# Kernel tuning notes

Measured on AMD Instinct MI355X. Metric: run time of the kernel, lower is better.

## Reference

```python
import jax, jax.numpy as jnp
import numpy as np

# scaled DeepSeek-V2-style config
B, S, D, H, L = 1, 2048, 1024, 16, 2
E, K, I, SI, V = 8, 2, 512, 1024, 32000
Dh = D // H
IGNORE_IDX = -100


def setup_inputs() -> dict:
    key = jax.random.key(0)
    ks = jax.random.split(key, 18)
    f = lambda k, sh: jax.random.normal(k, sh, jnp.float32) * 0.02
    return {
        "src_tokens": jax.random.randint(ks[0], (B, S), 0, V, jnp.int32),
        "target": jax.random.randint(ks[1], (B, S), 0, V, jnp.int32),
        "embed": f(ks[2], (V, D)),
        "Wq": f(ks[3], (L, D, D)),
        "Wk": f(ks[4], (L, D, D)),
        "Wv": f(ks[5], (L, D, D)),
        "Wo": f(ks[6], (L, D, D)),
        "ln1": jnp.ones((L, D), jnp.float32),
        "ln2": jnp.ones((L, D), jnp.float32),
        "gate_w": f(ks[7], (L, E, D)),
        "gate_projs": f(ks[8], (L, E, I, D)),
        "up_projs": f(ks[9], (L, E, I, D)),
        "down_projs": f(ks[10], (L, E, D, I)),
        "sg": f(ks[11], (L, SI, D)),
        "su": f(ks[12], (L, SI, D)),
        "sd": f(ks[13], (L, D, SI)),
        "final_ln": jnp.ones((D,), jnp.float32),
        "lm_head": f(ks[14], (V, D)),
    }


def _rms(x, w, eps=1e-6):
    return x * jax.lax.rsqrt(jnp.mean(x * x, axis=-1, keepdims=True) + eps) * w


def _rot_half(x):
    x1, x2 = jnp.split(x, 2, axis=-1)
    return jnp.concatenate([-x2, x1], axis=-1)


def reference(src_tokens, target, embed, Wq, Wk, Wv, Wo, ln1, ln2, gate_w,
              gate_projs, up_projs, down_projs, sg, su, sd, final_ln, lm_head):
    # rotary tables [1,S,1,Dh]
    inv_freq = 1.0 / (10000.0 ** (jnp.arange(0, Dh, 2, dtype=jnp.float32) / Dh))
    ang = jnp.arange(S, dtype=jnp.float32)[:, None] * inv_freq[None, :]
    emb = jnp.concatenate([ang, ang], axis=-1)
    cos = jnp.cos(emb)[None, :, None, :]
    sin = jnp.sin(emb)[None, :, None, :]
    causal = jnp.tril(jnp.ones((S, S), bool))
    scale = 1.0 / float(np.sqrt(Dh))

    h = embed[src_tokens]  # [B,S,D]
    for l in range(L):
        x = _rms(h, ln1[l])
        q = (x @ Wq[l].T).reshape(B, S, H, Dh)
        k = (x @ Wk[l].T).reshape(B, S, H, Dh)
        v = (x @ Wv[l].T).reshape(B, S, H, Dh)
        q = q * cos + _rot_half(q) * sin
        k = k * cos + _rot_half(k) * sin
        sc = jnp.einsum('bqhd,bkhd->bhqk', q, k) * scale
        sc = jnp.where(causal, sc, -1e9)
        a = jax.nn.softmax(sc, axis=-1)
        o = jnp.einsum('bhqk,bkhd->bqhd', a, v).reshape(B, S, D)
        h = h + o @ Wo[l].T
        # DeepSeek-V2 MoE: softmax gate -> top-k combine over stacked experts
        x = _rms(h, ln2[l])
        probs = jax.nn.softmax(x @ gate_w[l].T, axis=-1)  # [B,S,E]
        topv, topi = jax.lax.top_k(probs, K)
        comb = (jax.nn.one_hot(topi, E, dtype=x.dtype) * topv[..., None]).sum(axis=2)  # [B,S,E]
        g = jnp.einsum('bsd,eid->bsei', x, gate_projs[l])
        u = jnp.einsum('bsd,eid->bsei', x, up_projs[l])
        act = jax.nn.silu(g) * u * comb[..., None]  # [B,S,E,I]
        routed = jnp.einsum('bsei,edi->bsd', act, down_projs[l])
        shared = (jax.nn.silu(x @ sg[l].T) * (x @ su[l].T)) @ sd[l].T
        h = h + routed + shared

    x = _rms(h, final_ln)
    logits = (x @ lm_head.T).reshape(-1, V).astype(jnp.float32)
    labels = target.reshape(-1)
    logp = jax.nn.log_softmax(logits, axis=-1)
    valid = labels != IGNORE_IDX
    safe = jnp.where(valid, labels, 0)
    nll = -jnp.take_along_axis(logp, safe[:, None], axis=1)[:, 0]
    loss = jnp.sum(jnp.where(valid, nll, 0.0))
    return loss
```

## Files before the change

kernel.cpp:

```cpp
#include <hip/hip_runtime.h>
#include <hip/hip_bf16.h>

#define S 2048
#define D 1024
#define H 16
#define DH 64
#define LAYERS 2
#define E 8
#define I_DIM 512
#define SI 1024
#define V 32000
#define NSTRIP 125

typedef unsigned short ushort_t;
typedef __attribute__((ext_vector_type(8))) short short8;
typedef __attribute__((ext_vector_type(4))) float floatx4;

__device__ __forceinline__ float bf2f(ushort_t u) {
  union { unsigned i; float f; } x;
  x.i = ((unsigned)u) << 16;
  return x.f;
}
__device__ __forceinline__ ushort_t f2bf(float f) {
  union { float f; unsigned u; } x; x.f = f;
  unsigned r = x.u + 0x7FFFu + ((x.u >> 16) & 1u);
  return (ushort_t)(r >> 16);
}
__device__ __forceinline__ int pack2(float a, float b) {
  return (int)((unsigned)f2bf(a) | ((unsigned)f2bf(b) << 16));
}

__device__ __forceinline__ int xcd_swz(int bid, int nwg) {
  int q = nwg >> 3, r = nwg & 7;
  int x = bid & 7, o = bid >> 3;
  return (x < r ? x * (q + 1) : r * (q + 1) + (x - r) * q) + o;
}

__device__ __forceinline__ void gl_lds16(const ushort_t* g, ushort_t* l) {
  __builtin_amdgcn_global_load_lds((const __attribute__((address_space(1))) void*)g,
                                   (__attribute__((address_space(3))) void*)l, 16, 0, 0);
}

__global__ __launch_bounds__(256) void convert_k(const float* __restrict__ in,
                                                 ushort_t* __restrict__ out, int n8) {
  int i = blockIdx.x * 256 + threadIdx.x;
  if (i >= n8) return;
  const float4* p = (const float4*)in + (size_t)i * 2;
  float4 a = p[0], b = p[1];
  int4 pk = {pack2(a.x, a.y), pack2(a.z, a.w), pack2(b.x, b.y), pack2(b.z, b.w)};
  ((int4*)out)[i] = pk;
}

__global__ __launch_bounds__(256) void convert_ilv_k(const float* __restrict__ in,
                                                     ushort_t* __restrict__ out,
                                                     int n8, int off) {
  int i = blockIdx.x * 256 + threadIdx.x;
  if (i >= n8) return;
  int row = i >> 7;
  int c8 = i & 127;
  const float4* p = (const float4*)in + (size_t)i * 2;
  float4 a = p[0], b = p[1];
  int4 pk = {pack2(a.x, a.y), pack2(a.z, a.w), pack2(b.x, b.y), pack2(b.z, b.w)};
  ((int4*)(out + ((size_t)(2 * row + off)) * D))[c8] = pk;
}

__global__ __launch_bounds__(256) void embed_k(const int* __restrict__ tok,
                                               const float* __restrict__ emb,
                                               float* __restrict__ h) {
  int idx = blockIdx.x * 256 + threadIdx.x;
  if (idx >= S * D / 4) return;
  int s = idx >> 8;
  int d4 = idx & 255;
  int t = tok[s];
  float4 u = *(const float4*)(emb + (size_t)t * D + d4 * 4);
  *(float4*)(h + (size_t)s * D + d4 * 4) = u;
}

__global__ __launch_bounds__(256) void rmsnorm_k(const float* __restrict__ h,
                                                 const float* __restrict__ w,
                                                 ushort_t* __restrict__ xb) {
  int s = blockIdx.x, tid = threadIdx.x;
  __shared__ float red[256];
  float4 hv = *(const float4*)(h + (size_t)s * D + tid * 4);
  red[tid] = hv.x * hv.x + hv.y * hv.y + hv.z * hv.z + hv.w * hv.w;
  __syncthreads();
  for (int st = 128; st > 0; st >>= 1) {
    if (tid < st) red[tid] += red[tid + st];
    __syncthreads();
  }
  float inv = rsqrtf(red[0] * (1.0f / 1024.0f) + 1e-6f);
  float4 wv = *(const float4*)(w + tid * 4);
  int2 pk;
  pk.x = pack2(hv.x * inv * wv.x, hv.y * inv * wv.y);
  pk.y = pack2(hv.z * inv * wv.z, hv.w * inv * wv.w);
  *(int2*)(xb + (size_t)s * D + tid * 4) = pk;
}

template <int TM, int TN, int MODE, int EXPERT>
__global__ __launch_bounds__(256) void gbt_k(const ushort_t* __restrict__ A, int lda,
                                             const ushort_t* __restrict__ B, int ldb,
                                             void* __restrict__ Cv, int ldc, int K) {
  constexpr int WM = TM / 2, WN = TN / 2;
  constexpr int MT = WM / 16, NT = WN / 16;
  constexpr int CA = TM / 16, CB = TN / 16;
  __shared__ __align__(16) ushort_t As[TM * 32];
  __shared__ __align__(16) ushort_t Bs[TN * 32];
  int tid = threadIdx.x;
  int nwg = gridDim.x * gridDim.y;
  int sw = xcd_swz(blockIdx.x + gridDim.x * blockIdx.y, nwg);
  int bx = sw / gridDim.y, by = sw % gridDim.y;
  int n0 = bx * TN, m0 = by * TM;
  int w = tid >> 6, lane = tid & 63, quad = lane >> 4, l16 = lane & 15;
  int wm = (w >> 1) * WM, wn = (w & 1) * WN;
  int srow = lane >> 2, sko = (lane & 3) * 8;

  floatx4 acc[MT][NT];
#pragma unroll
  for (int mi = 0; mi < MT; mi++)
#pragma unroll
    for (int ni = 0; ni < NT; ni++)
      acc[mi][ni] = (floatx4){0.f, 0.f, 0.f, 0.f};

  for (int k0 = 0; k0 < K; k0 += 32) {
#pragma unroll
    for (int c = 0; c < CA; c += 4) {
      int ch = c + w;
      const ushort_t* gp = A + (size_t)(m0 + ch * 16 + srow) * lda + k0 + sko;
      gl_lds16(gp, As + ch * 512);
    }
#pragma unroll
    for (int c = 0; c < CB; c += 4) {
      int ch = c + w;
      const ushort_t* gp;
      if (EXPERT) {
        int kk = k0 + sko;
        int e = kk >> 9;
        gp = B + ((size_t)(e * D + n0 + ch * 16 + srow)) * I_DIM + (kk & 511);
      } else {
        gp = B + (size_t)(n0 + ch * 16 + srow) * ldb + k0 + sko;
      }
      gl_lds16(gp, Bs + ch * 512);
    }
    __syncthreads();
    short8 af[MT], bfv[NT];
#pragma unroll
    for (int mi = 0; mi < MT; mi++)
      af[mi] = *(const short8*)(As + (wm + mi * 16 + l16) * 32 + quad * 8);
#pragma unroll
    for (int ni = 0; ni < NT; ni++)
      bfv[ni] = *(const short8*)(Bs + (wn + ni * 16 + l16) * 32 + quad * 8);
#pragma unroll
    for (int mi = 0; mi < MT; mi++)
#pragma unroll
      for (int ni = 0; ni < NT; ni++)
        acc[mi][ni] = __builtin_amdgcn_mfma_f32_16x16x32_bf16(af[mi], bfv[ni],
                                                              acc[mi][ni], 0, 0, 0);
    __syncthreads();
  }
#pragma unroll
  for (int mi = 0; mi < MT; mi++) {
#pragma unroll
    for (int ni = 0; ni < NT; ni++) {
      int row_base = m0 + wm + mi * 16 + quad * 4;
      int col = n0 + wn + ni * 16 + l16;
#pragma unroll
      for (int r = 0; r < 4; r++) {
        if (MODE == 1) {
          ((ushort_t*)Cv)[(size_t)(row_base + r) * ldc + col] = f2bf(acc[mi][ni][r]);
        } else if (MODE == 3) {
          float g = acc[mi][ni][r];
          float u = __shfl_xor(g, 1);
          if (!(l16 & 1)) {
            float sig = 1.0f / (1.0f + __expf(-g));
            ((ushort_t*)Cv)[(size_t)(row_base + r) * ldc + (col >> 1)] =
                f2bf(g * sig * u);
          }
        } else {
          float* cp = (float*)Cv + (size_t)(row_base + r) * ldc + col;
          float val = acc[mi][ni][r];
          if (MODE == 2) val += *cp;
          *cp = val;
        }
      }
    }
  }
}

#define GBODY(T, VMSTR, DOSTAGE)                                              \
  {                                                                           \
    if (DOSTAGE) STAGE((T) + 1);                                              \
    asm volatile("s_waitcnt vmcnt(" VMSTR ")" ::: "memory");                  \
    __builtin_amdgcn_sched_barrier(0);                                        \
    __builtin_amdgcn_s_barrier();                                             \
    __builtin_amdgcn_sched_barrier(0);                                        \
    asm volatile("" ::: "memory");                                            \
    const ushort_t* bA = smem + ((T) & 1) * SLOT;                             \
    const ushort_t* bB = bA + TM2 * 32;                                       \
    short8 af[MT], bfv[4];                                                    \
    _Pragma("unroll") for (int mi = 0; mi < MT; mi++) {                       \
      int row = wm + mi * 16 + l16;                                           \
      af[mi] = *(const short8*)(bA + row * 32 + ((quad ^ ((row >> 1) & 3)) << 3)); \
    }                                                                         \
    _Pragma("unroll") for (int ni = 0; ni < 4; ni++) {                        \
      int row = wn + ni * 16 + l16;                                           \
      bfv[ni] = *(const short8*)(bB + row * 32 + ((quad ^ ((row >> 1) & 3)) << 3)); \
    }                                                                         \
    __builtin_amdgcn_s_setprio(1);                                            \
    _Pragma("unroll") for (int mi = 0; mi < MT; mi++)                         \
      _Pragma("unroll") for (int ni = 0; ni < 4; ni++)                        \
        acc[mi][ni] = __builtin_amdgcn_mfma_f32_16x16x32_bf16(                \
            af[mi], bfv[ni], acc[mi][ni], 0, 0, 0);                           \
    __builtin_amdgcn_s_setprio(0);                                            \
    __builtin_amdgcn_sched_barrier(0);                                        \
    __builtin_amdgcn_s_barrier();                                             \
    asm volatile("" ::: "memory");                                            \
  }

template <int TM2, int MODE>
__global__ __launch_bounds__(512, 2) void gemm256_k(
    const ushort_t* __restrict__ A, int lda,
    const ushort_t* __restrict__ B, int ldb,
    void* __restrict__ Cv, int ldc, int K,
    const int* __restrict__ target, float2* __restrict__ partial,
    float* __restrict__ tgt_l, const float* __restrict__ combp, int strip_base) {
  constexpr int MT = TM2 / 32;
  constexpr int SLOT = (TM2 + 256) * 32;
  constexpr int RA = TM2 / 128;
  __shared__ __align__(16) ushort_t smem[2 * SLOT];
  int tid = threadIdx.x;
  int wv = tid >> 6, lane = tid & 63, quad = lane >> 4, l16 = lane & 15;
  int wm = (wv >> 2) * (TM2 / 2), wn = (wv & 3) * 64;
  int nwg = gridDim.x * gridDim.y;
  int sw = xcd_swz(blockIdx.x + gridDim.x * blockIdx.y, nwg);
  int bx = sw / gridDim.y, by = sw % gridDim.y;
  int m0 = by * TM2, n0 = bx * 256;
  int NT = K / 32;

  floatx4 acc[MT][4];
#pragma unroll
  for (int mi = 0; mi < MT; mi++)
#pragma unroll
    for (int ni = 0; ni < 4; ni++) acc[mi][ni] = (floatx4){0.f, 0.f, 0.f, 0.f};

  auto STAGE = [&](int t) {
    int b = t & 1, k0 = t * 32;
    ushort_t* ba = smem + b * SLOT;
#pragma unroll
    for (int ra = 0; ra < RA; ra++) {
      int Pb = ra * 8192 + tid * 16;
      int row = Pb >> 6;
      int kq = ((Pb >> 4) & 3) ^ ((row >> 1) & 3);
      gl_lds16(A + (size_t)(m0 + row) * lda + k0 + kq * 8,
               ba + ((ra * 8192 + wv * 1024) >> 1));
    }
#pragma unroll
    for (int rb = 0; rb < 2; rb++) {
      int Pb = rb * 8192 + tid * 16;
      int row = Pb >> 6;
      int kq = ((Pb >> 4) & 3) ^ ((row >> 1) & 3);
      gl_lds16(B + (size_t)(n0 + row) * ldb + k0 + kq * 8,
               ba + TM2 * 32 + ((rb * 8192 + wv * 1024) >> 1));
    }
  };

  STAGE(0);
  if constexpr (RA == 2) {
    for (int t = 0; t < NT - 1; t++) GBODY(t, "4", 1);
    GBODY(NT - 1, "0", 0);
  } else {
    for (int t = 0; t < NT - 1; t++) GBODY(t, "3", 1);
    GBODY(NT - 1, "0", 0);
  }

  if constexpr (MODE == 0) {
    ushort_t* C = (ushort_t*)Cv;
#pragma unroll
    for (int mi = 0; mi < MT; mi++)
#pragma unroll
      for (int ni = 0; ni < 4; ni++) {
        int rb = m0 + wm + mi * 16 + quad * 4;
        int col = n0 + wn + ni * 16 + l16;
#pragma unroll
        for (int r = 0; r < 4; r++)
          C[(size_t)(rb + r) * ldc + col] = f2bf(acc[mi][ni][r]);
      }
  } else if constexpr (MODE == 2) {
    float* cb = (float*)smem;
    int e = n0 >> 10;
    if (tid < TM2) cb[tid] = combp[(size_t)(m0 + tid) * E + e];
    __syncthreads();
    ushort_t* Cp = (ushort_t*)Cv;
#pragma unroll
    for (int mi = 0; mi < MT; mi++)
#pragma unroll
      for (int ni = 0; ni < 4; ni++) {
        int lrow = wm + mi * 16 + quad * 4;
        int colg = n0 + wn + ni * 16 + l16;
#pragma unroll
        for (int r = 0; r < 4; r++) {
          float g = acc[mi][ni][r];
          float u = __shfl_xor(g, 1);
          if (!(l16 & 1)) {
            float sig = 1.0f / (1.0f + __expf(-g));
            Cp[(size_t)(m0 + lrow + r) * 4096 + (colg >> 1)] =
                f2bf(g * sig * u * cb[lrow + r]);
          }
        }
      }
  } else {
    int strip = strip_base + bx;
    int n0g = strip * 256;
    float* pm = (float*)smem;
    float* pl = pm + TM2 * 4;
    int* tg = (int*)(pl + TM2 * 4);
    if (tid < TM2) tg[tid] = target[m0 + tid];
    __syncthreads();
#pragma unroll
    for (int mi = 0; mi < MT; mi++) {
      float rmax[4], rsum[4];
#pragma unroll
      for (int r = 0; r < 4; r++) {
        float m = acc[mi][0][r];
#pragma unroll
        for (int ni = 1; ni < 4; ni++) m = fmaxf(m, acc[mi][ni][r]);
        rmax[r] = m;
      }
#pragma unroll
      for (int msk = 1; msk <= 8; msk <<= 1)
#pragma unroll
        for (int r = 0; r < 4; r++)
          rmax[r] = fmaxf(rmax[r], __shfl_xor(rmax[r], msk));
#pragma unroll
      for (int r = 0; r < 4; r++) {
        float ssum = 0.f;
#pragma unroll
        for (int ni = 0; ni < 4; ni++) ssum += __expf(acc[mi][ni][r] - rmax[r]);
        rsum[r] = ssum;
      }
#pragma unroll
      for (int msk = 1; msk <= 8; msk <<= 1)
#pragma unroll
        for (int r = 0; r < 4; r++) rsum[r] += __shfl_xor(rsum[r], msk);
      int rib = wm + mi * 16 + quad * 4;
#pragma unroll
      for (int r = 0; r < 4; r++) {
        int tt = tg[rib + r];
#pragma unroll
        for (int ni = 0; ni < 4; ni++) {
          int colg = n0g + wn + ni * 16 + l16;
          if (tt == colg) tgt_l[m0 + rib + r] = acc[mi][ni][r];
        }
      }
      if (l16 == 0) {
#pragma unroll
        for (int r = 0; r < 4; r++) {
          pm[(rib + r) * 4 + (wv & 3)] = rmax[r];
          pl[(rib + r) * 4 + (wv & 3)] = rsum[r];
        }
      }
    }
    __syncthreads();
    if (tid < TM2) {
      float m = pm[tid * 4];
#pragma unroll
      for (int j = 1; j < 4; j++) m = fmaxf(m, pm[tid * 4 + j]);
      float l = 0.f;
#pragma unroll
      for (int j = 0; j < 4; j++) l += pl[tid * 4 + j] * __expf(pm[tid * 4 + j] - m);
      partial[(size_t)(m0 + tid) * NSTRIP + strip] = make_float2(m, l);
    }
  }
}

__global__ __launch_bounds__(256) void reduce_lse_k(const float2* __restrict__ partial,
                                                    const int* __restrict__ target,
                                                    const float* __restrict__ tgt_l,
                                                    float* __restrict__ nll) {
  int row = blockIdx.x * 256 + threadIdx.x;
  if (row >= S) return;
  float m = -1e30f, l = 0.f;
  for (int j = 0; j < NSTRIP; j++) {
    float2 pp = partial[(size_t)row * NSTRIP + j];
    float nm = fmaxf(m, pp.x);
    l = l * __expf(m - nm) + pp.y * __expf(pp.x - nm);
    m = nm;
  }
  int t = target[row];
  nll[row] = (t != -100) ? (logf(l) + m - tgt_l[row]) : 0.f;
}

__global__ __launch_bounds__(256) void sum_nll_k(const float* __restrict__ nll,
                                                 float* __restrict__ out) {
  __shared__ float red[256];
  int tid = threadIdx.x;
  float acc = 0.f;
  for (int s = tid; s < S; s += 256) acc += nll[s];
  red[tid] = acc;
  __syncthreads();
  for (int st = 128; st > 0; st >>= 1) {
    if (tid < st) red[tid] += red[tid + st];
    __syncthreads();
  }
  if (tid == 0) out[0] = red[0];
}

__global__ __launch_bounds__(256) void rope_tab_k(float2* __restrict__ tab) {
  int idx = blockIdx.x * 256 + threadIdx.x;
  int s = idx >> 5, i = idx & 31;
  float invf = expf(-(float)i * (9.210340371976184f / 32.0f));
  float ang = (float)s * invf;
  tab[idx] = make_float2(cosf(ang), sinf(ang));
}

__global__ __launch_bounds__(256) void rope_k(ushort_t* __restrict__ qkv,
                                              const float2* __restrict__ tab) {
  int idx = blockIdx.x * 256 + threadIdx.x;
  int s = idx >> 9;
  int r = idx & 511;
  int hd = r >> 5, i = r & 31;
  float2 cs = tab[(s << 5) | i];
  float c = cs.x, sn = cs.y;
  size_t base = (size_t)s * 3072 + hd * DH + i;
  float q1 = bf2f(qkv[base]), q2 = bf2f(qkv[base + 32]);
  qkv[base] = f2bf(q1 * c - q2 * sn);
  qkv[base + 32] = f2bf(q2 * c + q1 * sn);
  float k1 = bf2f(qkv[base + 1024]), k2 = bf2f(qkv[base + 1024 + 32]);
  qkv[base + 1024] = f2bf(k1 * c - k2 * sn);
  qkv[base + 1024 + 32] = f2bf(k2 * c + k1 * sn);
}

#define PSTR 72
__global__ __launch_bounds__(256) void flash_attn_k(const ushort_t* __restrict__ q,
                                                    const ushort_t* __restrict__ k,
                                                    const ushort_t* __restrict__ v,
                                                    ushort_t* __restrict__ out) {
  __shared__ __align__(16) ushort_t QPs[64 * PSTR];
  __shared__ __align__(16) ushort_t Ks[64 * PSTR];
  __shared__ __align__(16) ushort_t Vt[64 * PSTR];
  int nwg = gridDim.x * gridDim.y;
  int sw = xcd_swz(blockIdx.x + gridDim.x * blockIdx.y, nwg);
  int hh = sw / gridDim.x;
  int qt = (gridDim.x - 1) - (sw % gridDim.x);
  int q0 = qt * 64;
  int tid = threadIdx.x;
  int w = tid >> 6, lane = tid & 63, quad = lane >> 4, l16 = lane & 15;

  {
    int row = tid >> 2, c0 = (tid & 3) * 16;
    const ushort_t* p = q + (size_t)(q0 + row) * 3072 + hh * DH + c0;
    *(int4*)(QPs + row * PSTR + c0) = ((const int4*)p)[0];
    *(int4*)(QPs + row * PSTR + c0 + 8) = ((const int4*)p)[1];
  }
  __syncthreads();
  short8 af[2];
  af[0] = *(const short8*)(QPs + (w * 16 + l16) * PSTR + quad * 8);
  af[1] = *(const short8*)(QPs + (w * 16 + l16) * PSTR + 32 + quad * 8);

  float m_i[4], l_i[4];
  floatx4 oacc[4];
#pragma unroll
  for (int r = 0; r < 4; r++) { m_i[r] = -1e30f; l_i[r] = 0.f; }
#pragma unroll
  for (int ni = 0; ni < 4; ni++) oacc[ni] = (floatx4){0.f, 0.f, 0.f, 0.f};

  for (int kt = 0; kt <= qt; kt++) {
    int kb = kt * 64;
    __syncthreads();
    {
      int row = tid >> 2, c0 = (tid & 3) * 16;
      const ushort_t* p = k + (size_t)(kb + row) * 3072 + hh * DH + c0;
      *(int4*)(Ks + row * PSTR + c0) = ((const int4*)p)[0];
      *(int4*)(Ks + row * PSTR + c0 + 8) = ((const int4*)p)[1];
    }
    {
      const ushort_t* p = v + (size_t)(kb + lane) * 3072 + hh * DH + w * 16;
      ushort_t tmp[16];
      *(int4*)tmp = ((const int4*)p)[0];
      *(int4*)(tmp + 8) = ((const int4*)p)[1];
#pragma unroll
      for (int j = 0; j < 16; j++)
        Vt[(w * 16 + j) * PSTR + lane] = tmp[j];
    }
    __syncthreads();
    floatx4 sfr[4];
#pragma unroll
    for (int ni = 0; ni < 4; ni++) sfr[ni] = (floatx4){0.f, 0.f, 0.f, 0.f};
#pragma unroll
    for (int ks = 0; ks < 2; ks++) {
#pragma unroll
      for (int ni = 0; ni < 4; ni++) {
        short8 bfr = *(const short8*)(Ks + (ni * 16 + l16) * PSTR + ks * 32 + quad * 8);
        sfr[ni] = __builtin_amdgcn_mfma_f32_16x16x32_bf16(af[ks], bfr, sfr[ni], 0, 0, 0);
      }
    }
    int qrow = q0 + w * 16 + quad * 4;
#pragma unroll
    for (int ni = 0; ni < 4; ni++) {
#pragma unroll
      for (int r = 0; r < 4; r++) {
        float s = sfr[ni][r] * 0.125f;
        if (kt == qt) {
          int key = kb + ni * 16 + l16;
          if (key > qrow + r) s = -1e30f;
        }
        sfr[ni][r] = s;
      }
    }
    float tmax[4];
#pragma unroll
    for (int r = 0; r < 4; r++)
      tmax[r] = fmaxf(fmaxf(sfr[0][r], sfr[1][r]), fmaxf(sfr[2][r], sfr[3][r]));
#pragma unroll
    for (int msk = 1; msk <= 8; msk <<= 1)
#pragma unroll
      for (int r = 0; r < 4; r++)
        tmax[r] = fmaxf(tmax[r], __shfl_xor(tmax[r], msk));
    float alpha[4];
#pragma unroll
    for (int r = 0; r < 4; r++) {
      float mn = fmaxf(m_i[r], tmax[r]);
      alpha[r] = __expf(m_i[r] - mn);
      m_i[r] = mn;
    }
    float tsum[4] = {0.f, 0.f, 0.f, 0.f};
#pragma unroll
    for (int ni = 0; ni < 4; ni++) {
#pragma unroll
      for (int r = 0; r < 4; r++) {
        float p = __expf(sfr[ni][r] - m_i[r]);
        sfr[ni][r] = p;
        tsum[r] += p;
      }
    }
#pragma unroll
    for (int msk = 1; msk <= 8; msk <<= 1)
#pragma unroll
      for (int r = 0; r < 4; r++)
        tsum[r] += __shfl_xor(tsum[r], msk);
#pragma unroll
    for (int r = 0; r < 4; r++) l_i[r] = l_i[r] * alpha[r] + tsum[r];
#pragma unroll
    for (int ni = 0; ni < 4; ni++)
#pragma unroll
      for (int r = 0; r < 4; r++) oacc[ni][r] *= alpha[r];
#pragma unroll
    for (int ni = 0; ni < 4; ni++)
#pragma unroll
      for (int r = 0; r < 4; r++)
        QPs[(w * 16 + quad * 4 + r) * PSTR + ni * 16 + l16] = f2bf(sfr[ni][r]);
    __threadfence_block();
#pragma unroll
    for (int ks = 0; ks < 2; ks++) {
      short8 pf = *(const short8*)(QPs + (w * 16 + l16) * PSTR + ks * 32 + quad * 8);
#pragma unroll
      for (int ni = 0; ni < 4; ni++) {
        short8 bfr = *(const short8*)(Vt + (ni * 16 + l16) * PSTR + ks * 32 + quad * 8);
        oacc[ni] = __builtin_amdgcn_mfma_f32_16x16x32_bf16(pf, bfr, oacc[ni], 0, 0, 0);
      }
    }
  }
#pragma unroll
  for (int r = 0; r < 4; r++) l_i[r] = 1.0f / l_i[r];
#pragma unroll
  for (int ni = 0; ni < 4; ni++) {
#pragma unroll
    for (int r = 0; r < 4; r++) {
      int row = q0 + w * 16 + quad * 4 + r;
      out[(size_t)row * D + hh * DH + ni * 16 + l16] = f2bf(oacc[ni][r] * l_i[r]);
    }
  }
}

__global__ __launch_bounds__(256) void gate_top2_k(const ushort_t* __restrict__ x,
                                                   const float* __restrict__ gw,
                                                   float* __restrict__ comb) {
  int s = blockIdx.x, tid = threadIdx.x;
  __shared__ float xs[D];
  __shared__ float red[E][32];
  __shared__ float lg[E];
  for (int i = tid; i < D; i += 256) xs[i] = bf2f(x[(size_t)s * D + i]);
  __syncthreads();
  int e = tid >> 5, j = tid & 31;
  float p = 0.f;
  for (int d = j; d < D; d += 32) p += xs[d] * gw[e * D + d];
  red[e][j] = p;
  __syncthreads();
  if (tid < E) {
    float sum = 0.f;
    for (int jj = 0; jj < 32; jj++) sum += red[tid][jj];
    lg[tid] = sum;
  }
  __syncthreads();
  if (tid == 0) {
    float m = lg[0];
    for (int i = 1; i < E; i++) m = fmaxf(m, lg[i]);
    float pr[E];
    float ssum = 0.f;
    for (int i = 0; i < E; i++) { pr[i] = __expf(lg[i] - m); ssum += pr[i]; }
    float rs = 1.0f / ssum;
    for (int i = 0; i < E; i++) pr[i] *= rs;
    int b1 = 0;
    for (int i = 1; i < E; i++) if (pr[i] > pr[b1]) b1 = i;
    int b2 = -1;
    for (int i = 0; i < E; i++) {
      if (i == b1) continue;
      if (b2 < 0 || pr[i] > pr[b2]) b2 = i;
    }
    for (int i = 0; i < E; i++)
      comb[(size_t)s * E + i] = (i == b1) ? pr[b1] : ((i == b2) ? pr[b2] : 0.f);
  }
}

extern "C" void kernel_launch(void* const* d_in, const int* in_sizes, int n_in,
                              void* d_out, int out_size, void* d_ws, size_t ws_size,
                              hipStream_t stream) {
  const int* src_tokens   = (const int*)d_in[0];
  const int* target       = (const int*)d_in[1];
  const float* embed      = (const float*)d_in[2];
  const float* Wq         = (const float*)d_in[3];
  const float* Wk         = (const float*)d_in[4];
  const float* Wv         = (const float*)d_in[5];
  const float* Wo         = (const float*)d_in[6];
  const float* ln1        = (const float*)d_in[7];
  const float* ln2        = (const float*)d_in[8];
  const float* gate_w     = (const float*)d_in[9];
  const float* gate_projs = (const float*)d_in[10];
  const float* up_projs   = (const float*)d_in[11];
  const float* down_projs = (const float*)d_in[12];
  const float* sg         = (const float*)d_in[13];
  const float* su         = (const float*)d_in[14];
  const float* sd         = (const float*)d_in[15];
  const float* final_ln   = (const float*)d_in[16];
  const float* lm_head    = (const float*)d_in[17];
  float* out = (float*)d_out;

  const size_t SD = (size_t)S * D;
  char* p = (char*)d_ws;
  float* h        = (float*)p;    p += SD * 4;
  ushort_t* qkvb  = (ushort_t*)p; p += (size_t)S * 3072 * 2;
  ushort_t* xb    = (ushort_t*)p; p += SD * 2;
  ushort_t* aob   = (ushort_t*)p; p += SD * 2;
  ushort_t* gu    = (ushort_t*)p; p += (size_t)S * 8192 * 2;
  ushort_t* act_bf= (ushort_t*)p; p += (size_t)S * 4096 * 2;
  ushort_t* xgu   = (ushort_t*)p; p += (size_t)S * 2048 * 2;
  float* comb     = (float*)p;    p += (size_t)S * E * 4;
  float* tgt_l    = (float*)p;    p += S * 4;
  float* nll      = (float*)p;    p += S * 4;
  float2* partial = (float2*)p;   p += (size_t)S * NSTRIP * 8;
  float2* rtab    = (float2*)p;   p += (size_t)S * 32 * 8;
  ushort_t* qkv_w = (ushort_t*)p; p += (size_t)LAYERS * 3072 * D * 2;
  ushort_t* Wo_bf = (ushort_t*)p; p += (size_t)LAYERS * D * D * 2;
  ushort_t* gu_w  = (ushort_t*)p; p += (size_t)LAYERS * 8192 * D * 2;
  ushort_t* dp_bf = (ushort_t*)p; p += (size_t)LAYERS * E * D * I_DIM * 2;
  ushort_t* sgsu_w= (ushort_t*)p; p += (size_t)LAYERS * 2048 * D * 2;
  ushort_t* sd_bf = (ushort_t*)p; p += (size_t)LAYERS * D * SI * 2;
  ushort_t* lmc   = gu;

  auto conv = [&](const float* src, ushort_t* dst, size_t n) {
    convert_k<<<(int)(n / 8 / 256), 256, 0, stream>>>(src, dst, (int)(n / 8));
  };
  const size_t DD = (size_t)D * D;
  for (int l = 0; l < LAYERS; l++) {
    conv(Wq + l * DD, qkv_w + (size_t)l * 3072 * D, DD);
    conv(Wk + l * DD, qkv_w + (size_t)l * 3072 * D + 1024 * D, DD);
    conv(Wv + l * DD, qkv_w + (size_t)l * 3072 * D + 2048 * D, DD);
    convert_ilv_k<<<(4096 * D / 8) / 256, 256, 0, stream>>>(
        gate_projs + (size_t)l * 4096 * D, gu_w + (size_t)l * 8192 * D, 4096 * D / 8, 0);
    convert_ilv_k<<<(4096 * D / 8) / 256, 256, 0, stream>>>(
        up_projs + (size_t)l * 4096 * D, gu_w + (size_t)l * 8192 * D, 4096 * D / 8, 1);
    convert_ilv_k<<<(1024 * D / 8) / 256, 256, 0, stream>>>(
        sg + (size_t)l * SI * D, sgsu_w + (size_t)l * 2048 * D, 1024 * D / 8, 0);
    convert_ilv_k<<<(1024 * D / 8) / 256, 256, 0, stream>>>(
        su + (size_t)l * SI * D, sgsu_w + (size_t)l * 2048 * D, 1024 * D / 8, 1);
  }
  conv(Wo, Wo_bf, LAYERS * DD);
  conv(down_projs, dp_bf, (size_t)LAYERS * E * D * I_DIM);
  conv(sd, sd_bf, (size_t)LAYERS * D * SI);

  rope_tab_k<<<(S * 32) / 256, 256, 0, stream>>>(rtab);
  embed_k<<<(S * D / 4) / 256, 256, 0, stream>>>(src_tokens, embed, h);

  for (int l = 0; l < LAYERS; l++) {
    rmsnorm_k<<<S, 256, 0, stream>>>(h, ln1 + (size_t)l * D, xb);
    gbt_k<128, 128, 1, 0><<<dim3(3072 / 128, S / 128), 256, 0, stream>>>(
        xb, D, qkv_w + (size_t)l * 3072 * D, D, qkvb, 3072, D);
    rope_k<<<(S * H * 32) / 256, 256, 0, stream>>>(qkvb, rtab);
    flash_attn_k<<<dim3(S / 64, H), 256, 0, stream>>>(qkvb, qkvb + 1024, qkvb + 2048, aob);
    gbt_k<64, 128, 2, 0><<<dim3(D / 128, S / 64), 256, 0, stream>>>(
        aob, D, Wo_bf + (size_t)l * DD, D, h, D, D);

    rmsnorm_k<<<S, 256, 0, stream>>>(h, ln2 + (size_t)l * D, xb);
    gate_top2_k<<<S, 256, 0, stream>>>(xb, gate_w + (size_t)l * E * D, comb);
    gemm256_k<128, 2><<<dim3(8192 / 256, S / 128), 512, 0, stream>>>(
        xb, D, gu_w + (size_t)l * 8192 * D, D, act_bf, 4096, D,
        nullptr, nullptr, nullptr, comb, 0);
    gbt_k<64, 128, 2, 1><<<dim3(D / 128, S / 64), 256, 0, stream>>>(
        act_bf, E * I_DIM, dp_bf + (size_t)l * E * D * I_DIM, 0, h, D, E * I_DIM);
    gbt_k<128, 128, 3, 0><<<dim3(2048 / 128, S / 128), 256, 0, stream>>>(
        xb, D, sgsu_w + (size_t)l * 2048 * D, D, xgu, 1024, D);
    gbt_k<64, 128, 2, 0><<<dim3(D / 128, S / 64), 256, 0, stream>>>(
        xgu, 1024, sd_bf + (size_t)l * D * SI, SI, h, D, SI);
  }

  rmsnorm_k<<<S, 256, 0, stream>>>(h, final_ln, xb);
  {
    conv(lm_head, lmc, (size_t)16384 * D);
    gemm256_k<256, 1><<<dim3(64, S / 256), 512, 0, stream>>>(
        xb, D, lmc, D, nullptr, 0, D, target, partial, tgt_l, nullptr, 0);
    conv(lm_head + (size_t)16384 * D, lmc, (size_t)15616 * D);
    gemm256_k<256, 1><<<dim3(61, S / 256), 512, 0, stream>>>(
        xb, D, lmc, D, nullptr, 0, D, target, partial, tgt_l, nullptr, 64);
  }
  reduce_lse_k<<<S / 256, 256, 0, stream>>>(partial, target, tgt_l, nll);
  sum_nll_k<<<1, 256, 0, stream>>>(nll, out);
}
```

Baseline: 1.248 ms.

## Replace 256-wide GEMM with 256x256x64 tile kernel using phased ping-pong LDS pipeline

Replaces the templated gemm256_k with g8_k, which uses a fixed 256x256 output tile, a K-step of 64 with an 8-way XOR swizzle, and splits each K-step into four MFMA phases. Global-to-LDS loads for the next B tile and the A tile two steps ahead are interleaved between phases. The MoE gate/up GEMM moves from 128-row to 256-row tiles, which halves its grid. The intent is to hide load latency behind MFMA work and raise data reuse, at the cost of more LDS (128KB), heavier register use at 2 waves per SIMD, and more barriers per step.

```diff
diff --git a/kernel.cpp b/kernel.cpp
--- a/kernel.cpp
+++ b/kernel.cpp
@@ -186,96 +186,165 @@
   }
 }
 
-#define GBODY(T, VMSTR, DOSTAGE)                                              \
-  {                                                                           \
-    if (DOSTAGE) STAGE((T) + 1);                                              \
-    asm volatile("s_waitcnt vmcnt(" VMSTR ")" ::: "memory");                  \
-    __builtin_amdgcn_sched_barrier(0);                                        \
-    __builtin_amdgcn_s_barrier();                                             \
-    __builtin_amdgcn_sched_barrier(0);                                        \
-    asm volatile("" ::: "memory");                                            \
-    const ushort_t* bA = smem + ((T) & 1) * SLOT;                             \
-    const ushort_t* bB = bA + TM2 * 32;                                       \
-    short8 af[MT], bfv[4];                                                    \
-    _Pragma("unroll") for (int mi = 0; mi < MT; mi++) {                       \
-      int row = wm + mi * 16 + l16;                                           \
-      af[mi] = *(const short8*)(bA + row * 32 + ((quad ^ ((row >> 1) & 3)) << 3)); \
-    }                                                                         \
-    _Pragma("unroll") for (int ni = 0; ni < 4; ni++) {                        \
-      int row = wn + ni * 16 + l16;                                           \
-      bfv[ni] = *(const short8*)(bB + row * 32 + ((quad ^ ((row >> 1) & 3)) << 3)); \
-    }                                                                         \
-    __builtin_amdgcn_s_setprio(1);                                            \
-    _Pragma("unroll") for (int mi = 0; mi < MT; mi++)                         \
-      _Pragma("unroll") for (int ni = 0; ni < 4; ni++)                        \
-        acc[mi][ni] = __builtin_amdgcn_mfma_f32_16x16x32_bf16(                \
-            af[mi], bfv[ni], acc[mi][ni], 0, 0, 0);                           \
-    __builtin_amdgcn_s_setprio(0);                                            \
-    __builtin_amdgcn_sched_barrier(0);                                        \
-    __builtin_amdgcn_s_barrier();                                             \
-    asm volatile("" ::: "memory");                                            \
-  }
-
-template <int TM2, int MODE>
-__global__ __launch_bounds__(512, 2) void gemm256_k(
+template <int MODE>
+__global__ __launch_bounds__(512, 2) void g8_k(
     const ushort_t* __restrict__ A, int lda,
     const ushort_t* __restrict__ B, int ldb,
     void* __restrict__ Cv, int ldc, int K,
     const int* __restrict__ target, float2* __restrict__ partial,
     float* __restrict__ tgt_l, const float* __restrict__ combp, int strip_base) {
-  constexpr int MT = TM2 / 32;
-  constexpr int SLOT = (TM2 + 256) * 32;
-  constexpr int RA = TM2 / 128;
-  __shared__ __align__(16) ushort_t smem[2 * SLOT];
+  __shared__ __align__(16) ushort_t smem[65536];
   int tid = threadIdx.x;
   int wv = tid >> 6, lane = tid & 63, quad = lane >> 4, l16 = lane & 15;
-  int wm = (wv >> 2) * (TM2 / 2), wn = (wv & 3) * 64;
+  int wm = (wv >> 2) * 128, wn = (wv & 3) * 64;
   int nwg = gridDim.x * gridDim.y;
   int sw = xcd_swz(blockIdx.x + gridDim.x * blockIdx.y, nwg);
   int bx = sw / gridDim.y, by = sw % gridDim.y;
-  int m0 = by * TM2, n0 = bx * 256;
-  int NT = K / 32;
-
-  floatx4 acc[MT][4];
-#pragma unroll
-  for (int mi = 0; mi < MT; mi++)
+  int m0 = by * 256, n0 = bx * 256;
+  int NT = K >> 6;
+
+  floatx4 acc[8][4];
+#pragma unroll
+  for (int mi = 0; mi < 8; mi++)
 #pragma unroll
     for (int ni = 0; ni < 4; ni++) acc[mi][ni] = (floatx4){0.f, 0.f, 0.f, 0.f};
 
-  auto STAGE = [&](int t) {
-    int b = t & 1, k0 = t * 32;
-    ushort_t* ba = smem + b * SLOT;
-#pragma unroll
-    for (int ra = 0; ra < RA; ra++) {
-      int Pb = ra * 8192 + tid * 16;
-      int row = Pb >> 6;
-      int kq = ((Pb >> 4) & 3) ^ ((row >> 1) & 3);
-      gl_lds16(A + (size_t)(m0 + row) * lda + k0 + kq * 8,
-               ba + ((ra * 8192 + wv * 1024) >> 1));
-    }
-#pragma unroll
-    for (int rb = 0; rb < 2; rb++) {
-      int Pb = rb * 8192 + tid * 16;
-      int row = Pb >> 6;
-      int kq = ((Pb >> 4) & 3) ^ ((row >> 1) & 3);
-      gl_lds16(B + (size_t)(n0 + row) * ldb + k0 + kq * 8,
-               ba + TM2 * 32 + ((rb * 8192 + wv * 1024) >> 1));
-    }
+  int srow = tid >> 3;
+  int sq = tid & 7;
+  auto STQ = [&](const ushort_t* X, int ldx, int x0, int k0, ushort_t* xb, int q) {
+    int r = q * 64 + srow;
+    int qg = sq ^ (r & 7);
+    gl_lds16(X + (size_t)(x0 + r) * ldx + k0 + qg * 8, xb + q * 4096 + wv * 512);
   };
-
-  STAGE(0);
-  if constexpr (RA == 2) {
-    for (int t = 0; t < NT - 1; t++) GBODY(t, "4", 1);
-    GBODY(NT - 1, "0", 0);
-  } else {
-    for (int t = 0; t < NT - 1; t++) GBODY(t, "3", 1);
-    GBODY(NT - 1, "0", 0);
-  }
+  auto LD = [&](const ushort_t* base, int r, int ks) -> short8 {
+    int qe = ks * 4 + quad;
+    return *(const short8*)(base + r * 64 + (((qe ^ (r & 7))) << 3));
+  };
+
+  {
+    ushort_t* b0A = smem;
+    ushort_t* b0B = smem + 16384;
+    ushort_t* b1A = smem + 32768;
+    STQ(A, lda, m0, 0, b0A, 0); STQ(A, lda, m0, 0, b0A, 1);
+    STQ(A, lda, m0, 0, b0A, 2); STQ(A, lda, m0, 0, b0A, 3);
+    STQ(B, ldb, n0, 0, b0B, 0); STQ(B, ldb, n0, 0, b0B, 1);
+    STQ(B, ldb, n0, 0, b0B, 2); STQ(B, ldb, n0, 0, b0B, 3);
+    if (NT > 1) {
+      STQ(A, lda, m0, 64, b1A, 0); STQ(A, lda, m0, 64, b1A, 1);
+      STQ(A, lda, m0, 64, b1A, 2); STQ(A, lda, m0, 64, b1A, 3);
+      asm volatile("s_waitcnt vmcnt(4)" ::: "memory");
+    } else {
+      asm volatile("s_waitcnt vmcnt(0)" ::: "memory");
+    }
+    __builtin_amdgcn_s_barrier();
+  }
+
+#define PH_SYNC()                                            \
+  __builtin_amdgcn_s_barrier();                              \
+  asm volatile("s_waitcnt lgkmcnt(0)" ::: "memory");         \
+  __builtin_amdgcn_sched_barrier(0);
+
+#define PH_END()                                             \
+  __builtin_amdgcn_s_setprio(0);                             \
+  __builtin_amdgcn_sched_barrier(0);                         \
+  __builtin_amdgcn_s_barrier();
+
+#pragma unroll 2
+  for (int t = 0; t < NT; t++) {
+    const int d = t & 1;
+    const ushort_t* bA = smem + d * 32768;
+    const ushort_t* bB = bA + 16384;
+    ushort_t* sB = smem + (d ^ 1) * 32768 + 16384;
+    ushort_t* sA = smem + d * 32768;
+    int k1 = (t + 1) << 6, k2 = (t + 2) << 6;
+    bool st1 = (t + 1) < NT, st2 = (t + 2) < NT;
+    short8 af[4][2], bf[2][2];
+
+#pragma unroll
+    for (int mi = 0; mi < 4; mi++)
+#pragma unroll
+      for (int ks = 0; ks < 2; ks++) af[mi][ks] = LD(bA, wm + mi * 16 + l16, ks);
+#pragma unroll
+    for (int ni = 0; ni < 2; ni++)
+#pragma unroll
+      for (int ks = 0; ks < 2; ks++) bf[ni][ks] = LD(bB, wn + ni * 16 + l16, ks);
+    if (st1) { STQ(B, ldb, n0, k1, sB, 0); STQ(B, ldb, n0, k1, sB, 1); }
+    PH_SYNC();
+    __builtin_amdgcn_s_setprio(1);
+#pragma unroll
+    for (int mi = 0; mi < 4; mi++)
+#pragma unroll
+      for (int ni = 0; ni < 2; ni++)
+#pragma unroll
+        for (int ks = 0; ks < 2; ks++)
+          acc[mi][ni] = __builtin_amdgcn_mfma_f32_16x16x32_bf16(
+              af[mi][ks], bf[ni][ks], acc[mi][ni], 0, 0, 0);
+    PH_END();
+
+#pragma unroll
+    for (int ni = 0; ni < 2; ni++)
+#pragma unroll
+      for (int ks = 0; ks < 2; ks++) bf[ni][ks] = LD(bB, wn + (ni + 2) * 16 + l16, ks);
+    if (st1) { STQ(B, ldb, n0, k1, sB, 2); STQ(B, ldb, n0, k1, sB, 3); }
+    PH_SYNC();
+    __builtin_amdgcn_s_setprio(1);
+#pragma unroll
+    for (int mi = 0; mi < 4; mi++)
+#pragma unroll
+      for (int ni = 0; ni < 2; ni++)
+#pragma unroll
+        for (int ks = 0; ks < 2; ks++)
+          acc[mi][ni + 2] = __builtin_amdgcn_mfma_f32_16x16x32_bf16(
+              af[mi][ks], bf[ni][ks], acc[mi][ni + 2], 0, 0, 0);
+    PH_END();
+
+#pragma unroll
+    for (int mi = 0; mi < 4; mi++)
+#pragma unroll
+      for (int ks = 0; ks < 2; ks++)
+        af[mi][ks] = LD(bA, wm + (mi + 4) * 16 + l16, ks);
+    if (st2) { STQ(A, lda, m0, k2, sA, 0); STQ(A, lda, m0, k2, sA, 2); }
+    PH_SYNC();
+    __builtin_amdgcn_s_setprio(1);
+#pragma unroll
+    for (int mi = 0; mi < 4; mi++)
+#pragma unroll
+      for (int ni = 0; ni < 2; ni++)
+#pragma unroll
+        for (int ks = 0; ks < 2; ks++)
+          acc[mi + 4][ni + 2] = __builtin_amdgcn_mfma_f32_16x16x32_bf16(
+              af[mi][ks], bf[ni][ks], acc[mi + 4][ni + 2], 0, 0, 0);
+    PH_END();
+
+#pragma unroll
+    for (int ni = 0; ni < 2; ni++)
+#pragma unroll
+      for (int ks = 0; ks < 2; ks++) bf[ni][ks] = LD(bB, wn + ni * 16 + l16, ks);
+    if (st2) { STQ(A, lda, m0, k2, sA, 1); STQ(A, lda, m0, k2, sA, 3); }
+    if (t < NT - 2) {
+      asm volatile("s_waitcnt vmcnt(4)" ::: "memory");
+    } else if (t == NT - 2) {
+      asm volatile("s_waitcnt vmcnt(0)" ::: "memory");
+    }
+    PH_SYNC();
+    __builtin_amdgcn_s_setprio(1);
+#pragma unroll
+    for (int mi = 0; mi < 4; mi++)
+#pragma unroll
+      for (int ni = 0; ni < 2; ni++)
+#pragma unroll
+        for (int ks = 0; ks < 2; ks++)
+          acc[mi + 4][ni] = __builtin_amdgcn_mfma_f32_16x16x32_bf16(
+              af[mi][ks], bf[ni][ks], acc[mi + 4][ni], 0, 0, 0);
+    PH_END();
+  }
+#undef PH_SYNC
+#undef PH_END
 
   if constexpr (MODE == 0) {
     ushort_t* C = (ushort_t*)Cv;
 #pragma unroll
-    for (int mi = 0; mi < MT; mi++)
+    for (int mi = 0; mi < 8; mi++)
 #pragma unroll
       for (int ni = 0; ni < 4; ni++) {
         int rb = m0 + wm + mi * 16 + quad * 4;
@@ -287,11 +356,11 @@
   } else if constexpr (MODE == 2) {
     float* cb = (float*)smem;
     int e = n0 >> 10;
-    if (tid < TM2) cb[tid] = combp[(size_t)(m0 + tid) * E + e];
+    if (tid < 256) cb[tid] = combp[(size_t)(m0 + tid) * E + e];
     __syncthreads();
     ushort_t* Cp = (ushort_t*)Cv;
 #pragma unroll
-    for (int mi = 0; mi < MT; mi++)
+    for (int mi = 0; mi < 8; mi++)
 #pragma unroll
       for (int ni = 0; ni < 4; ni++) {
         int lrow = wm + mi * 16 + quad * 4;
@@ -311,12 +380,12 @@
     int strip = strip_base + bx;
     int n0g = strip * 256;
     float* pm = (float*)smem;
-    float* pl = pm + TM2 * 4;
-    int* tg = (int*)(pl + TM2 * 4);
-    if (tid < TM2) tg[tid] = target[m0 + tid];
-    __syncthreads();
-#pragma unroll
-    for (int mi = 0; mi < MT; mi++) {
+    float* pl = pm + 1024;
+    int* tg = (int*)(pl + 1024);
+    if (tid < 256) tg[tid] = target[m0 + tid];
+    __syncthreads();
+#pragma unroll
+    for (int mi = 0; mi < 8; mi++) {
       float rmax[4], rsum[4];
 #pragma unroll
       for (int r = 0; r < 4; r++) {
@@ -360,7 +429,7 @@
       }
     }
     __syncthreads();
-    if (tid < TM2) {
+    if (tid < 256) {
       float m = pm[tid * 4];
 #pragma unroll
       for (int j = 1; j < 4; j++) m = fmaxf(m, pm[tid * 4 + j]);
@@ -691,7 +760,7 @@
 
     rmsnorm_k<<<S, 256, 0, stream>>>(h, ln2 + (size_t)l * D, xb);
     gate_top2_k<<<S, 256, 0, stream>>>(xb, gate_w + (size_t)l * E * D, comb);
-    gemm256_k<128, 2><<<dim3(8192 / 256, S / 128), 512, 0, stream>>>(
+    g8_k<2><<<dim3(8192 / 256, S / 256), 512, 0, stream>>>(
         xb, D, gu_w + (size_t)l * 8192 * D, D, act_bf, 4096, D,
         nullptr, nullptr, nullptr, comb, 0);
     gbt_k<64, 128, 2, 1><<<dim3(D / 128, S / 64), 256, 0, stream>>>(
@@ -705,10 +774,10 @@
   rmsnorm_k<<<S, 256, 0, stream>>>(h, final_ln, xb);
   {
     conv(lm_head, lmc, (size_t)16384 * D);
-    gemm256_k<256, 1><<<dim3(64, S / 256), 512, 0, stream>>>(
+    g8_k<1><<<dim3(64, S / 256), 512, 0, stream>>>(
         xb, D, lmc, D, nullptr, 0, D, target, partial, tgt_l, nullptr, 0);
     conv(lm_head + (size_t)16384 * D, lmc, (size_t)15616 * D);
-    gemm256_k<256, 1><<<dim3(61, S / 256), 512, 0, stream>>>(
+    g8_k<1><<<dim3(61, S / 256), 512, 0, stream>>>(
         xb, D, lmc, D, nullptr, 0, D, target, partial, tgt_l, nullptr, 64);
   }
   reduce_lse_k<<<S / 256, 256, 0, stream>>>(partial, target, tgt_l, nll);
```

New measurement: 1.253 ms. About the same (+0.4%).
